# Performance work log

Hardware: AMD Instinct MI355X
Metric: run time of the kernel (lower is better)

## Reference

```python
import jax, jax.numpy as jnp
import numpy as np

B, NA, D, LS1, H, A = 16384, 5, 128, 128, 128, 64

# com_k consumes observations in the order used by torch.stack in forward
PERM = np.array([[1,2,3,4,0],[0,2,3,4,1],[0,1,3,4,2],[0,1,2,4,3],[0,1,2,3,4]])
# TIDX[agent, lstm] = which com time-step feeds agent's dense2 input
TIDX = np.array([[4,0,0,0,0],[0,4,1,1,1],[1,1,4,2,2],[2,2,2,4,3],[3,3,3,3,4]])


def _lstm_step(x, h, c, Wih, Whh, bih, bhh):
    # x: [L,B,in], h/c: [L,B,H]; Wih: [L,4H,in], Whh: [L,4H,H]; torch gate order i,f,g,o
    gates = (jnp.einsum('lbf,lgf->lbg', x, Wih)
             + jnp.einsum('lbh,lgh->lbg', h, Whh)
             + (bih + bhh)[:, None, :])
    i, f, g, o = jnp.split(gates, 4, axis=-1)
    c2 = jax.nn.sigmoid(f) * c + jax.nn.sigmoid(i) * jnp.tanh(g)
    h2 = jax.nn.sigmoid(o) * jnp.tanh(c2)
    return h2, c2


def setup_inputs() -> dict:
    key = jax.random.key(0)
    ks = jax.random.split(key, 16)
    s1 = float(1.0 / np.sqrt(D))
    sh = float(1.0 / np.sqrt(H))
    s2 = float(1.0 / np.sqrt(6 * H))
    f32 = jnp.float32
    return {
        'input': jax.random.normal(ks[0], (B, NA, D), f32),
        'h_0': jax.random.normal(ks[1], (NA, 1, B, H), f32),
        'c_0': jax.random.normal(ks[2], (NA, 1, B, H), f32),
        'd1_w': jax.random.normal(ks[3], (LS1, D), f32) * s1,
        'd1_b': jnp.zeros((LS1,), f32),
        'd2_w': jax.random.normal(ks[4], (A, 6 * H), f32) * s2,
        'd2_b': jnp.zeros((A,), f32),
        'mem_Wih': jax.random.normal(ks[5], (NA, 4 * H, LS1), f32) * sh,
        'mem_Whh': jax.random.normal(ks[6], (NA, 4 * H, H), f32) * sh,
        'mem_bih': jax.random.normal(ks[7], (NA, 4 * H), f32) * sh,
        'mem_bhh': jax.random.normal(ks[8], (NA, 4 * H), f32) * sh,
        'com_Wih': jax.random.normal(ks[9], (NA, 4 * H, LS1), f32) * sh,
        'com_Whh': jax.random.normal(ks[10], (NA, 4 * H, H), f32) * sh,
        'com_bih': jax.random.normal(ks[11], (NA, 4 * H), f32) * sh,
        'com_bhh': jax.random.normal(ks[12], (NA, 4 * H), f32) * sh,
    }


def reference(input, h_0, c_0, d1_w, d1_b, d2_w, d2_b,
              mem_Wih, mem_Whh, mem_bih, mem_bhh,
              com_Wih, com_Whh, com_bih, com_bhh):
    Bn = input.shape[0]
    # shared dense1 applied to all 5 agent observations: [NA, B, LS1]
    obs = jnp.einsum('bnd,od->nbo', input, d1_w) + d1_b
    # 5 memory LSTMs, seq_len == 1 -> a single batched cell step
    mem_h, mem_c = _lstm_step(obs, h_0[:, 0], c_0[:, 0], mem_Wih, mem_Whh, mem_bih, mem_bhh)
    # 5 com LSTMs over permuted 5-step sequences, zero initial state
    xs = jnp.swapaxes(obs[PERM], 0, 1)  # [T=5, L=5, B, LS1]
    z = jnp.zeros((NA, Bn, H), obs.dtype)

    def step(carry, x_t):
        h, c = carry
        h2, c2 = _lstm_step(x_t, h, c, com_Wih, com_Whh, com_bih, com_bhh)
        return (h2, c2), h2

    _, ys = jax.lax.scan(step, (z, z), xs)  # [T, L, B, H]
    # gather the cross-agent communication slices: sel[agent, lstm] = ys[TIDX[a,l], l]
    sel = ys[TIDX, np.arange(NA)[None, :]]  # [NA, NA, B, H]
    cat = jnp.concatenate(
        [jnp.transpose(sel, (0, 2, 1, 3)).reshape(NA, Bn, NA * H), mem_h], axis=-1)  # [NA,B,6H]
    outs = jnp.einsum('abf,of->abo', cat, d2_w) + d2_b  # [NA, B, A]
    h_n = mem_h[:, None]  # [NA, 1, B, H]
    c_n = mem_c[:, None]
    return (outs[0], outs[1], outs[2], outs[3], outs[4], h_n, c_n)
```

## Files before the change

kernel.cpp:

```cpp
#include <hip/hip_runtime.h>

#define BB   16384
#define NAg  5
#define DD   128
#define HH   128
#define G4   512
#define KC   256
#define AA   64
#define CATW 768

typedef __attribute__((ext_vector_type(8))) short bf16x8;
typedef __attribute__((ext_vector_type(4))) float f32x4;

#define DEV static __device__ __forceinline__

DEV unsigned short bf16r(float x){
  unsigned u = __float_as_uint(x);
  unsigned r = (u + 0x7fffu + ((u >> 16) & 1u)) >> 16;
  return (unsigned short)r;
}
DEV float sigf(float x){ return __builtin_amdgcn_rcpf(1.0f + __expf(-x)); }
DEV float tanhf_(float x){ return __builtin_fmaf(2.0f, __builtin_amdgcn_rcpf(1.0f + __expf(-2.0f * x)), -1.0f); }

DEV bf16x8 ld8(const unsigned short* p){ return *(const bf16x8*)p; }

DEV bf16x8 cvt8(const float* __restrict__ p){
  const float4* q = (const float4*)p;
  float4 v0 = q[0], v1 = q[1];
  bf16x8 r;
  r[0]=(short)bf16r(v0.x); r[1]=(short)bf16r(v0.y); r[2]=(short)bf16r(v0.z); r[3]=(short)bf16r(v0.w);
  r[4]=(short)bf16r(v1.x); r[5]=(short)bf16r(v1.y); r[6]=(short)bf16r(v1.z); r[7]=(short)bf16r(v1.w);
  return r;
}

__global__ void k_prep(const float* __restrict__ d1w, const float* __restrict__ d2w,
                       const float* __restrict__ mWih, const float* __restrict__ mWhh,
                       const float* __restrict__ mbih, const float* __restrict__ mbhh,
                       const float* __restrict__ cWih, const float* __restrict__ cWhh,
                       const float* __restrict__ cbih, const float* __restrict__ cbhh,
                       unsigned short* d1w_bf, unsigned short* d2w_bf,
                       unsigned short* Wm, unsigned short* Wc, float* bm, float* bc)
{
  const long long TOT = 16384 + 49152 + 655360 + 655360 + 2560 + 2560;
  for (long long i = (long long)blockIdx.x * 256 + threadIdx.x; i < TOT;
       i += (long long)gridDim.x * 256) {
    long long x = i;
    if (x < 16384) { d1w_bf[x] = bf16r(d1w[x]); continue; }
    x -= 16384;
    if (x < 49152) { d2w_bf[x] = bf16r(d2w[x]); continue; }
    x -= 49152;
    if (x < 655360) {
      int e    = (int)(x & 7);
      int lane = (int)((x >> 3) & 63);
      int kt   = (int)((x >> 9) & 7);
      int q    = (int)((x >> 12) & 3);
      int w    = (int)((x >> 14) & 7);
      int n    = (int)(x >> 17);
      int g = q * 128 + w * 16 + (lane & 15);
      int k = kt * 32 + (lane >> 4) * 8 + e;
      Wm[x] = bf16r(k < 128 ? mWih[((size_t)n * 512 + g) * 128 + k]
                            : mWhh[((size_t)n * 512 + g) * 128 + (k - 128)]);
      continue;
    }
    x -= 655360;
    if (x < 655360) {
      int e    = (int)(x & 7);
      int lane = (int)((x >> 3) & 63);
      int kt   = (int)((x >> 9) & 7);
      int q    = (int)((x >> 12) & 3);
      int w    = (int)((x >> 14) & 7);
      int l0   = (int)(x >> 17);
      int g = q * 128 + w * 16 + (lane & 15);
      int k = kt * 32 + (lane >> 4) * 8 + e;
      Wc[x] = bf16r(k < 128 ? cWih[((size_t)l0 * 512 + g) * 128 + k]
                            : cWhh[((size_t)l0 * 512 + g) * 128 + (k - 128)]);
      continue;
    }
    x -= 655360;
    if (x < 2560) { bm[x] = mbih[x] + mbhh[x]; continue; }
    x -= 2560;
    bc[x] = cbih[x] + cbhh[x];
  }
}

__global__ __launch_bounds__(512) void k_memobs(const float* __restrict__ input,
                                                const unsigned short* __restrict__ d1w,
                                                const float* __restrict__ d1b,
                                                const float* __restrict__ h0,
                                                const float* __restrict__ c0,
                                                const unsigned short* __restrict__ Wmp,
                                                const float* __restrict__ bm,
                                                float* __restrict__ out_h,
                                                float* __restrict__ out_c,
                                                unsigned short* __restrict__ cat,
                                                unsigned short* __restrict__ obs_bf)
{
  __shared__ __align__(16) unsigned short os[64][128];
  __shared__ __align__(16) float hs[64][128];

  const int n = blockIdx.x >> 8;
  const int b0 = (blockIdx.x & 255) << 6;
  const int tid = threadIdx.x;
  const int w = tid >> 6, lane = tid & 63;
  const int c0l = lane & 15, hi = lane >> 4;
  const int u = w * 16 + c0l;

  const unsigned short* Wg = Wmp + (size_t)n * 131072 + (size_t)w * 16384 + lane * 8;

  const float biasD = d1b[u];
  f32x4 oacc[4];
  #pragma unroll
  for (int mt = 0; mt < 4; mt++) oacc[mt] = (f32x4){biasD, biasD, biasD, biasD};

  #pragma unroll
  for (int kt = 0; kt < 4; ++kt) {
    const int k = kt * 32 + hi * 8;
    bf16x8 bfrD = ld8(d1w + (size_t)u * DD + k);
    #pragma unroll
    for (int mt = 0; mt < 4; mt++) {
      const int br = b0 + mt * 16 + c0l;
      bf16x8 a = cvt8(input + ((size_t)br * NAg + n) * DD + k);
      oacc[mt] = __builtin_amdgcn_mfma_f32_16x16x32_bf16(a, bfrD, oacc[mt], 0, 0, 0);
    }
  }
  #pragma unroll
  for (int mt = 0; mt < 4; mt++) {
    #pragma unroll
    for (int j = 0; j < 4; j++) {
      const int r = mt * 16 + hi * 4 + j;
      os[r][u ^ ((r & 7) << 3)] = bf16r(oacc[mt][j]);
    }
  }
  __syncthreads();
  #pragma unroll
  for (int cc = 0; cc < 2; ++cc) {
    const int idx = cc * 512 + tid;
    const int r = idx >> 4;
    const int c8 = (idx & 15) << 3;
    bf16x8 v = *(const bf16x8*)&os[r][c8];
    *(bf16x8*)(obs_bf + ((size_t)n * BB + b0 + r) * DD + c8) = v;
  }

  const float bI = bm[n * G4 + u];
  const float bF = bm[n * G4 + 128 + u];
  const float bG = bm[n * G4 + 256 + u];
  const float bO = bm[n * G4 + 384 + u];

  float cnr[2][2][4];

  #pragma unroll
  for (int hh = 0; hh < 2; hh++) {
    f32x4 acc[2][4];
    #pragma unroll
    for (int m2 = 0; m2 < 2; m2++) {
      acc[m2][0] = (f32x4){bI, bI, bI, bI};
      acc[m2][1] = (f32x4){bF, bF, bF, bF};
      acc[m2][2] = (f32x4){bG, bG, bG, bG};
      acc[m2][3] = (f32x4){bO, bO, bO, bO};
    }

    #pragma unroll
    for (int kt = 0; kt < 8; ++kt) {
      bf16x8 bfr[4];
      #pragma unroll
      for (int q = 0; q < 4; q++) bfr[q] = ld8(Wg + (q * 8 + kt) * 512);
      bf16x8 a[2];
      #pragma unroll
      for (int m2 = 0; m2 < 2; m2++) {
        const int r = (hh * 2 + m2) * 16 + c0l;
        if (kt < 4) a[m2] = ld8(&os[r][(kt * 32 + hi * 8) ^ ((r & 7) << 3)]);
        else        a[m2] = cvt8(h0 + ((size_t)n * BB + b0 + r) * HH + (kt - 4) * 32 + hi * 8);
      }
      #pragma unroll
      for (int m2 = 0; m2 < 2; m2++)
        #pragma unroll
        for (int q = 0; q < 4; q++)
          acc[m2][q] = __builtin_amdgcn_mfma_f32_16x16x32_bf16(a[m2], bfr[q], acc[m2][q], 0, 0, 0);
    }

    #pragma unroll
    for (int m2 = 0; m2 < 2; m2++) {
      #pragma unroll
      for (int j = 0; j < 4; j++) {
        const int r = hh * 32 + m2 * 16 + hi * 4 + j;
        const float iv = acc[m2][0][j];
        const float fv = acc[m2][1][j];
        const float gv = acc[m2][2][j];
        const float ov = acc[m2][3][j];
        const float cold = c0[((size_t)n * BB + b0 + r) * HH + u];
        const float cn = sigf(fv) * cold + sigf(iv) * tanhf_(gv);
        const float hn = sigf(ov) * tanhf_(cn);
        cnr[hh][m2][j] = cn;
        hs[r][u ^ ((r & 7) << 3)] = hn;
      }
    }
  }
  __syncthreads();
  #pragma unroll
  for (int cc = 0; cc < 4; ++cc) {
    const int idx = cc * 512 + tid;
    const int r = idx >> 5;
    const int c4 = (idx & 31) << 2;
    float4 v = *(const float4*)&hs[r][c4 ^ ((r & 7) << 3)];
    *(float4*)(out_h + ((size_t)n * BB + b0 + r) * HH + c4) = v;
  }
  #pragma unroll
  for (int cc = 0; cc < 2; ++cc) {
    const int idx = cc * 512 + tid;
    const int r = idx >> 4;
    const int c8 = (idx & 15) << 3;
    const float* p = &hs[r][c8 ^ ((r & 7) << 3)];
    float4 v0 = *(const float4*)p, v1 = *(const float4*)(p + 4);
    bf16x8 bv;
    bv[0]=(short)bf16r(v0.x); bv[1]=(short)bf16r(v0.y); bv[2]=(short)bf16r(v0.z); bv[3]=(short)bf16r(v0.w);
    bv[4]=(short)bf16r(v1.x); bv[5]=(short)bf16r(v1.y); bv[6]=(short)bf16r(v1.z); bv[7]=(short)bf16r(v1.w);
    *(bf16x8*)(cat + ((size_t)n * BB + b0 + r) * CATW + 640 + c8) = bv;
  }
  __syncthreads();
  #pragma unroll
  for (int hh = 0; hh < 2; hh++)
    #pragma unroll
    for (int m2 = 0; m2 < 2; m2++)
      #pragma unroll
      for (int j = 0; j < 4; j++) {
        const int r = hh * 32 + m2 * 16 + hi * 4 + j;
        hs[r][u ^ ((r & 7) << 3)] = cnr[hh][m2][j];
      }
  __syncthreads();
  #pragma unroll
  for (int cc = 0; cc < 4; ++cc) {
    const int idx = cc * 512 + tid;
    const int r = idx >> 5;
    const int c4 = (idx & 31) << 2;
    float4 v = *(const float4*)&hs[r][c4 ^ ((r & 7) << 3)];
    *(float4*)(out_c + ((size_t)n * BB + b0 + r) * HH + c4) = v;
  }
}

__global__ __launch_bounds__(512) void k_comf(const unsigned short* __restrict__ obs_bf,
                                              const unsigned short* __restrict__ Wpk,
                                              const float* __restrict__ bc,
                                              unsigned short* __restrict__ cat)
{
  __shared__ __align__(16) unsigned short hl[2][64][128];
  __shared__ __align__(16) unsigned short ol[2][64][128];

  const int bid = blockIdx.x;
  const int swz = (bid & 7) * 160 + (bid >> 3);
  const int l0 = swz >> 8;
  const int b0 = (swz & 255) << 6;
  const int tid = threadIdx.x;
  const int w = tid >> 6, lane = tid & 63;
  const int c0l = lane & 15, hi = lane >> 4;
  const int u = w * 16 + c0l;

  const unsigned short* Wg = Wpk + (size_t)l0 * 131072 + (size_t)w * 16384 + lane * 8;
  bf16x8 wfr[4][8];
  #pragma unroll
  for (int q = 0; q < 4; q++)
    #pragma unroll
    for (int kt = 0; kt < 8; kt++)
      wfr[q][kt] = ld8(Wg + (q * 8 + kt) * 512);

  const float bI = bc[l0 * G4 + u];
  const float bF = bc[l0 * G4 + 128 + u];
  const float bG = bc[l0 * G4 + 256 + u];
  const float bO = bc[l0 * G4 + 384 + u];

  for (int i = tid; i < 8192; i += 512) ((unsigned short*)hl)[8192 + i] = 0;

  {
    const int it0 = (0 == 4) ? l0 : (0 + (0 >= l0 ? 1 : 0));
    const unsigned short* src = obs_bf + ((size_t)it0 * BB + b0) * DD;
    __builtin_amdgcn_global_load_lds((const unsigned int*)(src + tid * 8),
                                     (unsigned int*)((unsigned short*)ol + w * 512), 16, 0, 0);
    __builtin_amdgcn_global_load_lds((const unsigned int*)(src + 4096 + tid * 8),
                                     (unsigned int*)((unsigned short*)ol + 4096 + w * 512), 16, 0, 0);
  }
  __syncthreads();

  float creg[2][2][4];
  #pragma unroll
  for (int hh = 0; hh < 2; hh++)
    #pragma unroll
    for (int m2 = 0; m2 < 2; m2++)
      #pragma unroll
      for (int j = 0; j < 4; j++) creg[hh][m2][j] = 0.0f;

  for (int t = 0; t < 5; ++t) {
    const int it = (t == 4) ? l0 : (t + (t >= l0 ? 1 : 0));
    const int rbuf = (t + 1) & 1, wbuf = t & 1;
    const int ob_c = t & 1, ob_n = (t + 1) & 1;

    if (t < 4) {
      const int tn = t + 1;
      const int itn = (tn == 4) ? l0 : (tn + (tn >= l0 ? 1 : 0));
      const unsigned short* src = obs_bf + ((size_t)itn * BB + b0) * DD;
      unsigned short* dst = (unsigned short*)ol + ob_n * 8192 + w * 512;
      __builtin_amdgcn_global_load_lds((const unsigned int*)(src + tid * 8),
                                       (unsigned int*)dst, 16, 0, 0);
      __builtin_amdgcn_global_load_lds((const unsigned int*)(src + 4096 + tid * 8),
                                       (unsigned int*)(dst + 4096), 16, 0, 0);
    }

    #pragma unroll
    for (int hh = 0; hh < 2; hh++) {
      f32x4 acc[2][4];
      #pragma unroll
      for (int m2 = 0; m2 < 2; m2++) {
        acc[m2][0] = (f32x4){bI, bI, bI, bI};
        acc[m2][1] = (f32x4){bF, bF, bF, bF};
        acc[m2][2] = (f32x4){bG, bG, bG, bG};
        acc[m2][3] = (f32x4){bO, bO, bO, bO};
      }

      #pragma unroll
      for (int kt = 0; kt < 4; ++kt) {
        bf16x8 a[2];
        #pragma unroll
        for (int m2 = 0; m2 < 2; m2++) {
          const int r = (hh * 2 + m2) * 16 + c0l;
          a[m2] = ld8(&ol[ob_c][r][(kt * 32 + hi * 8) ^ ((r & 7) << 3)]);
        }
        #pragma unroll
        for (int m2 = 0; m2 < 2; m2++)
          #pragma unroll
          for (int q = 0; q < 4; q++)
            acc[m2][q] = __builtin_amdgcn_mfma_f32_16x16x32_bf16(a[m2], wfr[q][kt], acc[m2][q], 0, 0, 0);
      }

      if (hh == 0) __syncthreads();

      #pragma unroll
      for (int kt = 4; kt < 8; ++kt) {
        bf16x8 a[2];
        #pragma unroll
        for (int m2 = 0; m2 < 2; m2++) {
          const int r = (hh * 2 + m2) * 16 + c0l;
          a[m2] = ld8(&hl[rbuf][r][((kt - 4) * 32 + hi * 8) ^ ((r & 7) << 3)]);
        }
        #pragma unroll
        for (int m2 = 0; m2 < 2; m2++)
          #pragma unroll
          for (int q = 0; q < 4; q++)
            acc[m2][q] = __builtin_amdgcn_mfma_f32_16x16x32_bf16(a[m2], wfr[q][kt], acc[m2][q], 0, 0, 0);
      }

      #pragma unroll
      for (int m2 = 0; m2 < 2; m2++) {
        #pragma unroll
        for (int j = 0; j < 4; j++) {
          const int r = hh * 32 + m2 * 16 + hi * 4 + j;
          const float iv = acc[m2][0][j];
          const float fv = acc[m2][1][j];
          const float gv = acc[m2][2][j];
          const float ov = acc[m2][3][j];
          const float cn = sigf(fv) * creg[hh][m2][j] + sigf(iv) * tanhf_(gv);
          const float hn = sigf(ov) * tanhf_(cn);
          creg[hh][m2][j] = cn;
          hl[wbuf][r][u ^ ((r & 7) << 3)] = bf16r(hn);
        }
      }
    }
    __syncthreads();

    unsigned short* catb = cat + ((size_t)it * BB + b0) * CATW + l0 * 128;
    #pragma unroll
    for (int cc = 0; cc < 2; ++cc) {
      const int idx = cc * 512 + tid;
      const int r = idx >> 4;
      const int c8 = (idx & 15) << 3;
      bf16x8 v = *(const bf16x8*)&hl[wbuf][r][c8 ^ ((r & 7) << 3)];
      *(bf16x8*)(catb + (size_t)r * CATW + c8) = v;
    }
  }
}

__global__ __launch_bounds__(256) void k_d2(const unsigned short* __restrict__ cat,
                                            const unsigned short* __restrict__ d2w,
                                            const float* __restrict__ d2b,
                                            float* __restrict__ out)
{
  const int m0 = blockIdx.x * 128;
  const int w = threadIdx.x >> 6, l = threadIdx.x & 63;
  const int c0l = l & 15, hi = l >> 4;

  const unsigned short* arow0 = cat + (size_t)(m0 + w * 16 + c0l) * CATW;
  const unsigned short* arow1 = arow0 + (size_t)64 * CATW;
  f32x4 acc[2][4];
  #pragma unroll
  for (int mt = 0; mt < 2; mt++)
    #pragma unroll
    for (int nt = 0; nt < 4; nt++) acc[mt][nt] = (f32x4){0, 0, 0, 0};

  #pragma unroll 4
  for (int kt = 0; kt < 24; ++kt) {
    const int k = kt * 32 + hi * 8;
    bf16x8 a0 = ld8(arow0 + k);
    bf16x8 a1 = ld8(arow1 + k);
    #pragma unroll
    for (int nt = 0; nt < 4; nt++) {
      bf16x8 bfr = ld8(d2w + (size_t)(nt * 16 + c0l) * CATW + k);
      acc[0][nt] = __builtin_amdgcn_mfma_f32_16x16x32_bf16(a0, bfr, acc[0][nt], 0, 0, 0);
      acc[1][nt] = __builtin_amdgcn_mfma_f32_16x16x32_bf16(a1, bfr, acc[1][nt], 0, 0, 0);
    }
  }
  #pragma unroll
  for (int mt = 0; mt < 2; mt++) {
    #pragma unroll
    for (int nt = 0; nt < 4; nt++) {
      const int col = nt * 16 + c0l;
      const float bias = d2b[col];
      #pragma unroll
      for (int j = 0; j < 4; j++) {
        const int r = m0 + mt * 64 + w * 16 + hi * 4 + j;
        out[(size_t)r * AA + col] = acc[mt][nt][j] + bias;
      }
    }
  }
}

extern "C" void kernel_launch(void* const* d_in, const int* in_sizes, int n_in,
                              void* d_out, int out_size, void* d_ws, size_t ws_size,
                              hipStream_t stream)
{
  const float* input = (const float*)d_in[0];
  const float* h0    = (const float*)d_in[1];
  const float* c0    = (const float*)d_in[2];
  const float* d1w   = (const float*)d_in[3];
  const float* d1b   = (const float*)d_in[4];
  const float* d2w   = (const float*)d_in[5];
  const float* d2b   = (const float*)d_in[6];
  const float* mWih  = (const float*)d_in[7];
  const float* mWhh  = (const float*)d_in[8];
  const float* mbih  = (const float*)d_in[9];
  const float* mbhh  = (const float*)d_in[10];
  const float* cWih  = (const float*)d_in[11];
  const float* cWhh  = (const float*)d_in[12];
  const float* cbih  = (const float*)d_in[13];
  const float* cbhh  = (const float*)d_in[14];
  float* out = (float*)d_out;

  char* ws = (char*)d_ws;
  size_t off = 0;
  auto alloc = [&](size_t bytes) { void* p = ws + off; off += (bytes + 255) & ~255ull; return p; };
  unsigned short* d1w_bf = (unsigned short*)alloc(16384 * 2);
  unsigned short* d2w_bf = (unsigned short*)alloc(49152 * 2);
  unsigned short* Wm     = (unsigned short*)alloc(655360 * 2);
  unsigned short* Wcb    = (unsigned short*)alloc(655360 * 2);
  float* bm              = (float*)alloc(2560 * 4);
  float* bc              = (float*)alloc(2560 * 4);
  unsigned short* obs_bf = (unsigned short*)alloc((size_t)NAg * BB * DD * 2);
  unsigned short* cat    = (unsigned short*)alloc((size_t)NAg * BB * CATW * 2);

  float* out_h = out + (size_t)NAg * BB * AA;
  float* out_c = out_h + (size_t)NAg * BB * HH;

  k_prep<<<2048, 256, 0, stream>>>(d1w, d2w, mWih, mWhh, mbih, mbhh,
                                   cWih, cWhh, cbih, cbhh,
                                   d1w_bf, d2w_bf, Wm, Wcb, bm, bc);
  k_memobs<<<(NAg * BB) / 64, 512, 0, stream>>>(input, d1w_bf, d1b, h0, c0, Wm, bm,
                                                out_h, out_c, cat, obs_bf);
  k_comf<<<(NAg * BB) / 64, 512, 0, stream>>>(obs_bf, Wcb, bc, cat);
  k_d2<<<(NAg * BB) / 128, 256, 0, stream>>>(cat, d2w_bf, d2b, out);
}
```

Baseline: 348.8 us.

## Pre-convert h0 to swizzled bf16 and stage via direct LDS loads; hoist LSTM weights

The prep kernel now converts h_0 to bf16 in a swizzled layout. The memory-LSTM kernel loads each block's h_0 tile straight into shared memory with global_load_lds, instead of reading fp32 from global and converting inside the MMA loop. All 32 weight fragments per wave are also loaded once into registers before the loop, rather than per kt and per half. This removes the fp32 reads and conversion from the inner loop, but adds a full extra pass over h_0 in the prep kernel, 16 KB more shared memory per block, and a large rise in register pressure that may spill or lower occupancy.

Measured after the change: 316.4 us. 1.1x faster.

```diff
diff --git a/kernel.cpp b/kernel.cpp
--- a/kernel.cpp
+++ b/kernel.cpp
@@ -38,10 +38,12 @@
                        const float* __restrict__ mbih, const float* __restrict__ mbhh,
                        const float* __restrict__ cWih, const float* __restrict__ cWhh,
                        const float* __restrict__ cbih, const float* __restrict__ cbhh,
+                       const float* __restrict__ h0,
                        unsigned short* d1w_bf, unsigned short* d2w_bf,
-                       unsigned short* Wm, unsigned short* Wc, float* bm, float* bc)
+                       unsigned short* Wm, unsigned short* Wc, float* bm, float* bc,
+                       unsigned short* h0bf)
 {
-  const long long TOT = 16384 + 49152 + 655360 + 655360 + 2560 + 2560;
+  const long long TOT = 16384 + 49152 + 655360 + 655360 + 2560 + 2560 + 10485760ll;
   for (long long i = (long long)blockIdx.x * 256 + threadIdx.x; i < TOT;
        i += (long long)gridDim.x * 256) {
     long long x = i;
@@ -79,14 +81,20 @@
     x -= 655360;
     if (x < 2560) { bm[x] = mbih[x] + mbhh[x]; continue; }
     x -= 2560;
-    bc[x] = cbih[x] + cbhh[x];
+    if (x < 2560) { bc[x] = cbih[x] + cbhh[x]; continue; }
+    x -= 2560;
+    {
+      int d = (int)(x & 127);
+      int b = (int)((x >> 7) & 16383);
+      h0bf[(x - d) + (d ^ ((b & 7) << 3))] = bf16r(h0[x]);
+    }
   }
 }
 
 __global__ __launch_bounds__(512) void k_memobs(const float* __restrict__ input,
                                                 const unsigned short* __restrict__ d1w,
                                                 const float* __restrict__ d1b,
-                                                const float* __restrict__ h0,
+                                                const unsigned short* __restrict__ h0bf,
                                                 const float* __restrict__ c0,
                                                 const unsigned short* __restrict__ Wmp,
                                                 const float* __restrict__ bm,
@@ -96,6 +104,7 @@
                                                 unsigned short* __restrict__ obs_bf)
 {
   __shared__ __align__(16) unsigned short os[64][128];
+  __shared__ __align__(16) unsigned short hb[64][128];
   __shared__ __align__(16) float hs[64][128];
 
   const int n = blockIdx.x >> 8;
@@ -105,7 +114,21 @@
   const int c0l = lane & 15, hi = lane >> 4;
   const int u = w * 16 + c0l;
 
+  {
+    const unsigned short* src = h0bf + ((size_t)n * BB + b0) * DD;
+    __builtin_amdgcn_global_load_lds((const unsigned int*)(src + tid * 8),
+                                     (unsigned int*)((unsigned short*)hb + w * 512), 16, 0, 0);
+    __builtin_amdgcn_global_load_lds((const unsigned int*)(src + 4096 + tid * 8),
+                                     (unsigned int*)((unsigned short*)hb + 4096 + w * 512), 16, 0, 0);
+  }
+
   const unsigned short* Wg = Wmp + (size_t)n * 131072 + (size_t)w * 16384 + lane * 8;
+  bf16x8 wfr[4][8];
+  #pragma unroll
+  for (int q = 0; q < 4; q++)
+    #pragma unroll
+    for (int kt = 0; kt < 8; kt++)
+      wfr[q][kt] = ld8(Wg + (q * 8 + kt) * 512);
 
   const float biasD = d1b[u];
   f32x4 oacc[4];
@@ -161,21 +184,18 @@
 
     #pragma unroll
     for (int kt = 0; kt < 8; ++kt) {
-      bf16x8 bfr[4];
-      #pragma unroll
-      for (int q = 0; q < 4; q++) bfr[q] = ld8(Wg + (q * 8 + kt) * 512);
       bf16x8 a[2];
       #pragma unroll
       for (int m2 = 0; m2 < 2; m2++) {
         const int r = (hh * 2 + m2) * 16 + c0l;
         if (kt < 4) a[m2] = ld8(&os[r][(kt * 32 + hi * 8) ^ ((r & 7) << 3)]);
-        else        a[m2] = cvt8(h0 + ((size_t)n * BB + b0 + r) * HH + (kt - 4) * 32 + hi * 8);
+        else        a[m2] = ld8(&hb[r][((kt - 4) * 32 + hi * 8) ^ ((r & 7) << 3)]);
       }
       #pragma unroll
       for (int m2 = 0; m2 < 2; m2++)
         #pragma unroll
         for (int q = 0; q < 4; q++)
-          acc[m2][q] = __builtin_amdgcn_mfma_f32_16x16x32_bf16(a[m2], bfr[q], acc[m2][q], 0, 0, 0);
+          acc[m2][q] = __builtin_amdgcn_mfma_f32_16x16x32_bf16(a[m2], wfr[q][kt], acc[m2][q], 0, 0, 0);
     }
 
     #pragma unroll
@@ -452,14 +472,15 @@
   float* bc              = (float*)alloc(2560 * 4);
   unsigned short* obs_bf = (unsigned short*)alloc((size_t)NAg * BB * DD * 2);
   unsigned short* cat    = (unsigned short*)alloc((size_t)NAg * BB * CATW * 2);
+  unsigned short* h0bf   = (unsigned short*)alloc((size_t)NAg * BB * DD * 2);
 
   float* out_h = out + (size_t)NAg * BB * AA;
   float* out_c = out_h + (size_t)NAg * BB * HH;
 
   k_prep<<<2048, 256, 0, stream>>>(d1w, d2w, mWih, mWhh, mbih, mbhh,
-                                   cWih, cWhh, cbih, cbhh,
-                                   d1w_bf, d2w_bf, Wm, Wcb, bm, bc);
-  k_memobs<<<(NAg * BB) / 64, 512, 0, stream>>>(input, d1w_bf, d1b, h0, c0, Wm, bm,
+                                   cWih, cWhh, cbih, cbhh, h0,
+                                   d1w_bf, d2w_bf, Wm, Wcb, bm, bc, h0bf);
+  k_memobs<<<(NAg * BB) / 64, 512, 0, stream>>>(input, d1w_bf, d1b, h0bf, c0, Wm, bm,
                                                 out_h, out_c, cat, obs_bf);
   k_comf<<<(NAg * BB) / 64, 512, 0, stream>>>(obs_bf, Wcb, bc, cat);
   k_d2<<<(NAg * BB) / 128, 256, 0, stream>>>(cat, d2w_bf, d2b, out);
```
